# Kernel optimization log

Hardware: AMD Instinct MI355X
Metric: run time of the kernel (lower is better)

## Reference

```python
import jax, jax.numpy as jnp
import numpy as np
import math

D_PAIR = 64
N_HEADS = 4
D_HEAD = D_PAIR // N_HEADS


def setup_inputs() -> dict:
    key = jax.random.key(0)
    ks = jax.random.split(key, 9)
    B, L, D = 2, 256, D_PAIR
    s = 1.0 / math.sqrt(D)
    return {
        "z": jax.random.normal(ks[0], (B, L, L, D), dtype=jnp.float32),
        "ln_scale": jnp.ones((D,), jnp.float32),
        "ln_bias": jnp.zeros((D,), jnp.float32),
        "Wq": jax.random.normal(ks[1], (D, D), jnp.float32) * s,
        "Wk": jax.random.normal(ks[2], (D, D), jnp.float32) * s,
        "Wv": jax.random.normal(ks[3], (D, D), jnp.float32) * s,
        "Wg": jax.random.normal(ks[4], (D, D), jnp.float32) * s,
        "bg": jax.random.normal(ks[5], (D,), jnp.float32) * 0.02,
        "Wo": jax.random.normal(ks[6], (D, D), jnp.float32) * s,
        "bo": jax.random.normal(ks[7], (D,), jnp.float32) * 0.02,
    }


def _layernorm(x, scale, bias, eps=1e-5):
    mu = jnp.mean(x, axis=-1, keepdims=True)
    var = jnp.var(x, axis=-1, keepdims=True)
    return (x - mu) * jax.lax.rsqrt(var + eps) * scale + bias


def reference(z, ln_scale, ln_bias, Wq, Wk, Wv, Wg, bg, Wo, bo):
    B, L, _, D = z.shape
    H, Dh = N_HEADS, D_HEAD
    zn = _layernorm(z, ln_scale, ln_bias)
    # torch Linear(no bias): x @ W.T
    Q = (zn @ Wq.T).reshape(B, L, L, H, Dh)
    K = (zn @ Wk.T).reshape(B, L, L, H, Dh)
    V = (zn @ Wv.T).reshape(B, L, L, H, Dh)
    scale = 1.0 / math.sqrt(Dh)
    # row-wise attention: for each row l, attend over column index j
    attn = jnp.einsum("blihd,bljhd->blhij", Q, K) * scale  # [B,L,H,L,L]
    attn = jax.nn.softmax(attn, axis=-1)
    out = jnp.einsum("blhij,bljhd->blihd", attn, V).reshape(B, L, L, D)
    gate = jax.nn.sigmoid(zn @ Wg.T + bg)
    out = gate * out
    return out @ Wo.T + bo
```

## Files before the change

kernel.cpp:

```cpp
#include <hip/hip_runtime.h>
#include <hip/hip_bf16.h>
#include <math.h>


typedef __attribute__((ext_vector_type(4))) float f32x4;
typedef __attribute__((ext_vector_type(8))) short s16x8;
typedef __attribute__((ext_vector_type(4))) short s16x4;

#define MFMA16(a, b, c) __builtin_amdgcn_mfma_f32_16x16x32_bf16((a), (b), (c), 0, 0, 0)

__device__ __forceinline__ f32x4 mfma16b(s16x4 a, s16x4 b, f32x4 c) {
#if __has_builtin(__builtin_amdgcn_mfma_f32_16x16x16bf16_1k)
    return __builtin_amdgcn_mfma_f32_16x16x16bf16_1k(a, b, c, 0, 0, 0);
#elif __has_builtin(__builtin_amdgcn_mfma_f32_16x16x16_bf16)
    return __builtin_amdgcn_mfma_f32_16x16x16_bf16(a, b, c, 0, 0, 0);
#else
    f32x4 d;
    asm volatile("s_nop 1\n\t"
                 "v_mfma_f32_16x16x16_bf16 %0, %1, %2, %3\n\t"
                 "s_nop 7\n\t"
                 "s_nop 7"
                 : "=v"(d) : "v"(a), "v"(b), "v"(c));
    return d;
#endif
}

__device__ __forceinline__ float exp2a(float x) {
    float r;
    asm("v_exp_f32 %0, %1" : "=v"(r) : "v"(x));
    return r;
}
__device__ __forceinline__ float rcpa(float x) {
    float r;
    asm("v_rcp_f32 %0, %1" : "=v"(r) : "v"(x));
    return r;
}

__device__ __forceinline__ unsigned pk2(float a, float b) {
    union { __hip_bfloat162 h; unsigned u; } c;
    float2 t; t.x = a; t.y = b;
    c.h = __float22bfloat162_rn(t);
    return c.u;
}
__device__ __forceinline__ s16x8 cvt8(const float* p) {
    union { unsigned u[4]; s16x8 v; } r;
    r.u[0] = pk2(p[0], p[1]); r.u[1] = pk2(p[2], p[3]);
    r.u[2] = pk2(p[4], p[5]); r.u[3] = pk2(p[6], p[7]);
    return r.v;
}

static constexpr int WSLICE = 1024;
static constexpr int ZNL = 0;
static constexpr int KSH = 4096;
static constexpr int VT  = 9216;
static constexpr int LDS_EL = 13440;

__global__ __launch_bounds__(256, 3)
void ka_fused(const float* __restrict__ z, const float* __restrict__ ln_s,
              const float* __restrict__ ln_b, const float* __restrict__ Wq,
              const float* __restrict__ Wk, const float* __restrict__ Wv,
              const float* __restrict__ Wg, const float* __restrict__ bg,
              short* __restrict__ ws)
{
    __shared__ __align__(16) short lds[LDS_EL];
    const int tid = threadIdx.x, lane = tid & 63, w = tid >> 6;
    const int n16 = lane & 15, quad = lane >> 4;
    const int g = blockIdx.x, bl = g >> 2, h = g & 3;
    const size_t rowbase = (size_t)bl * (256 * 64);
    const int wsl = w * WSLICE;

    union { unsigned u[32]; s16x8 v8[8]; } row;
    {
        float zn[64];
        const float4* zp4 = (const float4*)(z + rowbase + (size_t)tid * 64);
        #pragma unroll
        for (int gq = 0; gq < 16; ++gq) {
            float4 v4 = zp4[gq];
            zn[gq * 4 + 0] = v4.x; zn[gq * 4 + 1] = v4.y;
            zn[gq * 4 + 2] = v4.z; zn[gq * 4 + 3] = v4.w;
        }
        float mu = 0.f;
        #pragma unroll
        for (int k = 0; k < 64; ++k) mu += zn[k];
        mu *= (1.f / 64.f);
        float va = 0.f;
        #pragma unroll
        for (int k = 0; k < 64; ++k) { float d = zn[k] - mu; va += d * d; }
        const float rs = rsqrtf(va * (1.f / 64.f) + 1e-5f);
        #pragma unroll
        for (int k = 0; k < 64; ++k) zn[k] = (zn[k] - mu) * rs * ln_s[k] + ln_b[k];
        #pragma unroll
        for (int k = 0; k < 32; ++k) row.u[k] = pk2(zn[2 * k], zn[2 * k + 1]);
    }

    auto store_row = [&]() {
        #pragma unroll
        for (int gq = 0; gq < 8; ++gq)
            *(s16x8*)&lds[ZNL + wsl + (lane & 15) * 64
                          + ((gq ^ (lane & 7)) * 8)] = row.v8[gq];
    };

    s16x8 bq[2], bk[2], bv[2], bgf[2];
    #pragma unroll
    for (int ks = 0; ks < 2; ++ks) {
        size_t off = (size_t)(h * 16 + n16) * 64 + ks * 32 + quad * 8;
        bq[ks] = cvt8(Wq + off);  bk[ks] = cvt8(Wk + off);
        bv[ks] = cvt8(Wv + off);  bgf[ks] = cvt8(Wg + off);
    }
    const float4 bg4 = *(const float4*)(bg + h * 16 + quad * 4);
    constexpr float QS  = 0.25f;
    constexpr float L2E = 1.44269504088896340736f;

    float g4t[4][4];
    s16x4 qa4[4];
    auto proj_tile = [&](int t) {
        s16x8 zn0 = *(const s16x8*)&lds[ZNL + wsl + n16 * 64
                                        + ((quad ^ (n16 & 7)) * 8)];
        s16x8 zn1 = *(const s16x8*)&lds[ZNL + wsl + n16 * 64
                                        + (((4 + quad) ^ (n16 & 7)) * 8)];
        f32x4 aq = {}, ak = {}, av = {}, ag = {};
        aq = MFMA16(bq[0], zn0, aq);  aq = MFMA16(bq[1], zn1, aq);
        ak = MFMA16(bk[0], zn0, ak);  ak = MFMA16(bk[1], zn1, ak);
        ag = MFMA16(bgf[0], zn0, ag); ag = MFMA16(bgf[1], zn1, ag);
        av = MFMA16(zn0, bv[0], av);  av = MFMA16(zn1, bv[1], av);
        {
            union { unsigned u[2]; s16x4 v; } q;
            q.u[0] = pk2(aq[0] * QS, aq[1] * QS);
            q.u[1] = pk2(aq[2] * QS, aq[3] * QS);
            qa4[t] = q.v;
        }
        {
            uint2 p = {pk2(ak[0], ak[1]), pk2(ak[2], ak[3])};
            *(uint2*)&lds[KSH + (w * 64 + t * 16 + n16) * 20 + quad * 4] = p;
        }
        {
            uint2 p = {pk2(av[0], av[1]), pk2(av[2], av[3])};
            *(uint2*)&lds[VT + n16 * 264 + (w * 64 + t * 16 + quad * 4)] = p;
        }
        #pragma unroll
        for (int r = 0; r < 4; ++r) {
            float x = ag[r] + bg4[r];
            g4t[t][r] = rcpa(1.f + exp2a(x * -L2E));
        }
    };

    if ((lane >> 4) == 0) store_row();
    proj_tile(0);
    if ((lane >> 4) == 1) store_row();
    proj_tile(1);
    if ((lane >> 4) == 2) store_row();
    proj_tile(2);
    if ((lane >> 4) == 3) store_row();
    proj_tile(3);
    __syncthreads();

    f32x4 o4[4], lacc[4];
    #pragma unroll
    for (int qt = 0; qt < 4; ++qt) { o4[qt] = {}; lacc[qt] = {}; }
    s16x4 ones4;
    {
        union { unsigned u[2]; s16x4 v; } c;
        c.u[0] = 0x3F803F80u; c.u[1] = 0x3F803F80u;
        ones4 = c.v;
    }
    const int kbase = KSH + n16 * 20 + quad * 4;
    const int vbase = VT + n16 * 264 + quad * 4;
    for (int ch = 0; ch < 8; ++ch) {
        #pragma unroll
        for (int jtl = 0; jtl < 2; ++jtl) {
            const int jt = ch * 2 + jtl;
            s16x4 kf = *(const s16x4*)&lds[kbase + jt * 320];
            s16x4 vf = *(const s16x4*)&lds[vbase + jt * 16];
            #pragma unroll
            for (int qt = 0; qt < 4; ++qt) {
                f32x4 zc = {};
                f32x4 s = mfma16b(kf, qa4[qt], zc);
                float e0 = exp2a(s[0] * L2E), e1 = exp2a(s[1] * L2E);
                float e2 = exp2a(s[2] * L2E), e3 = exp2a(s[3] * L2E);
                union { unsigned u[2]; s16x4 v; } pb;
                pb.u[0] = pk2(e0, e1); pb.u[1] = pk2(e2, e3);
                o4[qt]   = mfma16b(vf, pb.v, o4[qt]);
                lacc[qt] = mfma16b(ones4, pb.v, lacc[qt]);
            }
        }
    }

    #pragma unroll
    for (int qt = 0; qt < 4; ++qt) {
        const float l = (lacc[qt][0] + lacc[qt][1]) * 0.5f;
        const float inv = rcpa(l);
        float g0 = g4t[qt][0] * o4[qt][0] * inv;
        float g1 = g4t[qt][1] * o4[qt][1] * inv;
        float g2 = g4t[qt][2] * o4[qt][2] * inv;
        float g3 = g4t[qt][3] * o4[qt][3] * inv;
        uint2 p = {pk2(g0, g1), pk2(g2, g3)};
        short* dst = ws + (((size_t)h * 512 + bl) * 256 + w * 64 + qt * 16 + n16) * 16
                     + quad * 4;
        *(uint2*)dst = p;
    }
}

__global__ __launch_bounds__(256, 4)
void k3_out(const short* __restrict__ ws, const float* __restrict__ Wo,
            const float* __restrict__ bo, float* __restrict__ out)
{
    const int tid = threadIdx.x, lane = tid & 63, w = tid >> 6;
    const int n16 = lane & 15, quad = lane >> 4;
    const short* GO = ws;
    const int bl = blockIdx.x >> 1, half = blockIdx.x & 1;
    const int rowloc = half * 128 + w * 32;

    s16x8 bfr[4][2];
    #pragma unroll
    for (int nt = 0; nt < 4; ++nt)
        #pragma unroll
        for (int ks = 0; ks < 2; ++ks)
            bfr[nt][ks] = cvt8(Wo + (size_t)(nt * 16 + n16) * 64 + ks * 32 + quad * 8);

    f32x4 acc[2][4] = {};
    #pragma unroll
    for (int mt = 0; mt < 2; ++mt) {
        #pragma unroll
        for (int c = 0; c < 2; ++c) {
            int hp = c * 2 + (quad >> 1);
            const short* ap = &GO[(((size_t)hp * 512 + bl) * 256 + rowloc + mt * 16 + n16) * 16
                                  + (quad & 1) * 8];
            s16x8 a = *(const s16x8*)ap;
            #pragma unroll
            for (int nt = 0; nt < 4; ++nt)
                acc[mt][nt] = MFMA16(bfr[nt][c], a, acc[mt][nt]);
        }
    }
    #pragma unroll
    for (int nt = 0; nt < 4; ++nt) {
        const float4 b4 = *(const float4*)(bo + nt * 16 + quad * 4);
        f32x4 b4v; b4v[0] = b4.x; b4v[1] = b4.y; b4v[2] = b4.z; b4v[3] = b4.w;
        #pragma unroll
        for (int mt = 0; mt < 2; ++mt) {
            f32x4 v = acc[mt][nt] + b4v;
            *(f32x4*)&out[((size_t)bl * 256 + rowloc + mt * 16 + n16) * 64
                          + nt * 16 + quad * 4] = v;
        }
    }
}

extern "C" void kernel_launch(void* const* d_in, const int* in_sizes, int n_in,
                              void* d_out, int out_size, void* d_ws, size_t ws_size,
                              hipStream_t stream) {
    const float* z  = (const float*)d_in[0];
    const float* ls = (const float*)d_in[1];
    const float* lb = (const float*)d_in[2];
    const float* Wq = (const float*)d_in[3];
    const float* Wk = (const float*)d_in[4];
    const float* Wv = (const float*)d_in[5];
    const float* Wg = (const float*)d_in[6];
    const float* bg = (const float*)d_in[7];
    const float* Wo = (const float*)d_in[8];
    const float* bo = (const float*)d_in[9];
    float* out = (float*)d_out;
    short* wsp = (short*)d_ws;

    hipLaunchKernelGGL(ka_fused, dim3(2048), dim3(256), 0, stream,
                       z, ls, lb, Wq, Wk, Wv, Wg, bg, wsp);
    hipLaunchKernelGGL(k3_out, dim3(1024), dim3(256), 0, stream, wsp, Wo, bo, out);
}
```

Baseline: 149.8 us.

## Split LayerNorm into separate kernel writing bf16 normalized rows

Adds a k0_ln kernel that layer-normalizes each row once and stores it as bf16 in the output buffer, used as scratch. Before, each of the four head blocks re-read the fp32 z row and recomputed LayerNorm. The fused kernel now loads bf16 rows straight from global memory into the MFMA operands, drops the LDS staging area and reorders the block index so blocks for different heads of the same row sit farther apart. This cuts fp32 z traffic about fourfold and redundant LN math, at the cost of an extra launch and a bf16 round trip through global memory.

```diff
diff --git a/kernel.cpp b/kernel.cpp
--- a/kernel.cpp
+++ b/kernel.cpp
@@ -49,15 +49,43 @@
     return r.v;
 }
 
-static constexpr int WSLICE = 1024;
-static constexpr int ZNL = 0;
-static constexpr int KSH = 4096;
-static constexpr int VT  = 9216;
-static constexpr int LDS_EL = 13440;
+__global__ __launch_bounds__(256, 2)
+void k0_ln(const float* __restrict__ z, const float* __restrict__ ln_s,
+           const float* __restrict__ ln_b, short* __restrict__ znG)
+{
+    const size_t row = (size_t)blockIdx.x * 256 + threadIdx.x;
+    float zn[64];
+    const float4* zp4 = (const float4*)(z + row * 64);
+    #pragma unroll
+    for (int gq = 0; gq < 16; ++gq) {
+        float4 v4 = zp4[gq];
+        zn[gq * 4 + 0] = v4.x; zn[gq * 4 + 1] = v4.y;
+        zn[gq * 4 + 2] = v4.z; zn[gq * 4 + 3] = v4.w;
+    }
+    float mu = 0.f;
+    #pragma unroll
+    for (int k = 0; k < 64; ++k) mu += zn[k];
+    mu *= (1.f / 64.f);
+    float va = 0.f;
+    #pragma unroll
+    for (int k = 0; k < 64; ++k) { float d = zn[k] - mu; va += d * d; }
+    const float rs = rsqrtf(va * (1.f / 64.f) + 1e-5f);
+    #pragma unroll
+    for (int k = 0; k < 64; ++k) zn[k] = (zn[k] - mu) * rs * ln_s[k] + ln_b[k];
+    union { unsigned u[32]; uint4 q[8]; } pk;
+    #pragma unroll
+    for (int k = 0; k < 32; ++k) pk.u[k] = pk2(zn[2 * k], zn[2 * k + 1]);
+    uint4* dst = (uint4*)(znG + row * 64);
+    #pragma unroll
+    for (int i = 0; i < 8; ++i) dst[i] = pk.q[i];
+}
+
+static constexpr int KSH = 0;
+static constexpr int VT  = 5120;
+static constexpr int LDS_EL = 9344;
 
 __global__ __launch_bounds__(256, 3)
-void ka_fused(const float* __restrict__ z, const float* __restrict__ ln_s,
-              const float* __restrict__ ln_b, const float* __restrict__ Wq,
+void ka_fused(const short* __restrict__ znG, const float* __restrict__ Wq,
               const float* __restrict__ Wk, const float* __restrict__ Wv,
               const float* __restrict__ Wg, const float* __restrict__ bg,
               short* __restrict__ ws)
@@ -65,40 +93,8 @@
     __shared__ __align__(16) short lds[LDS_EL];
     const int tid = threadIdx.x, lane = tid & 63, w = tid >> 6;
     const int n16 = lane & 15, quad = lane >> 4;
-    const int g = blockIdx.x, bl = g >> 2, h = g & 3;
-    const size_t rowbase = (size_t)bl * (256 * 64);
-    const int wsl = w * WSLICE;
-
-    union { unsigned u[32]; s16x8 v8[8]; } row;
-    {
-        float zn[64];
-        const float4* zp4 = (const float4*)(z + rowbase + (size_t)tid * 64);
-        #pragma unroll
-        for (int gq = 0; gq < 16; ++gq) {
-            float4 v4 = zp4[gq];
-            zn[gq * 4 + 0] = v4.x; zn[gq * 4 + 1] = v4.y;
-            zn[gq * 4 + 2] = v4.z; zn[gq * 4 + 3] = v4.w;
-        }
-        float mu = 0.f;
-        #pragma unroll
-        for (int k = 0; k < 64; ++k) mu += zn[k];
-        mu *= (1.f / 64.f);
-        float va = 0.f;
-        #pragma unroll
-        for (int k = 0; k < 64; ++k) { float d = zn[k] - mu; va += d * d; }
-        const float rs = rsqrtf(va * (1.f / 64.f) + 1e-5f);
-        #pragma unroll
-        for (int k = 0; k < 64; ++k) zn[k] = (zn[k] - mu) * rs * ln_s[k] + ln_b[k];
-        #pragma unroll
-        for (int k = 0; k < 32; ++k) row.u[k] = pk2(zn[2 * k], zn[2 * k + 1]);
-    }
-
-    auto store_row = [&]() {
-        #pragma unroll
-        for (int gq = 0; gq < 8; ++gq)
-            *(s16x8*)&lds[ZNL + wsl + (lane & 15) * 64
-                          + ((gq ^ (lane & 7)) * 8)] = row.v8[gq];
-    };
+    const int g = blockIdx.x, bl = g & 511, h = g >> 9;
+    const int wsl_rows = w * 64;
 
     s16x8 bq[2], bk[2], bv[2], bgf[2];
     #pragma unroll
@@ -113,11 +109,12 @@
 
     float g4t[4][4];
     s16x4 qa4[4];
-    auto proj_tile = [&](int t) {
-        s16x8 zn0 = *(const s16x8*)&lds[ZNL + wsl + n16 * 64
-                                        + ((quad ^ (n16 & 7)) * 8)];
-        s16x8 zn1 = *(const s16x8*)&lds[ZNL + wsl + n16 * 64
-                                        + (((4 + quad) ^ (n16 & 7)) * 8)];
+    #pragma unroll
+    for (int t = 0; t < 4; ++t) {
+        const short* zr = znG + ((size_t)bl * 256 + wsl_rows + t * 16 + n16) * 64
+                          + quad * 8;
+        s16x8 zn0 = *(const s16x8*)zr;
+        s16x8 zn1 = *(const s16x8*)(zr + 32);
         f32x4 aq = {}, ak = {}, av = {}, ag = {};
         aq = MFMA16(bq[0], zn0, aq);  aq = MFMA16(bq[1], zn1, aq);
         ak = MFMA16(bk[0], zn0, ak);  ak = MFMA16(bk[1], zn1, ak);
@@ -131,27 +128,18 @@
         }
         {
             uint2 p = {pk2(ak[0], ak[1]), pk2(ak[2], ak[3])};
-            *(uint2*)&lds[KSH + (w * 64 + t * 16 + n16) * 20 + quad * 4] = p;
+            *(uint2*)&lds[KSH + (wsl_rows + t * 16 + n16) * 20 + quad * 4] = p;
         }
         {
             uint2 p = {pk2(av[0], av[1]), pk2(av[2], av[3])};
-            *(uint2*)&lds[VT + n16 * 264 + (w * 64 + t * 16 + quad * 4)] = p;
+            *(uint2*)&lds[VT + n16 * 264 + (wsl_rows + t * 16 + quad * 4)] = p;
         }
         #pragma unroll
         for (int r = 0; r < 4; ++r) {
             float x = ag[r] + bg4[r];
             g4t[t][r] = rcpa(1.f + exp2a(x * -L2E));
         }
-    };
-
-    if ((lane >> 4) == 0) store_row();
-    proj_tile(0);
-    if ((lane >> 4) == 1) store_row();
-    proj_tile(1);
-    if ((lane >> 4) == 2) store_row();
-    proj_tile(2);
-    if ((lane >> 4) == 3) store_row();
-    proj_tile(3);
+    }
     __syncthreads();
 
     f32x4 o4[4], lacc[4];
@@ -194,7 +182,7 @@
         float g2 = g4t[qt][2] * o4[qt][2] * inv;
         float g3 = g4t[qt][3] * o4[qt][3] * inv;
         uint2 p = {pk2(g0, g1), pk2(g2, g3)};
-        short* dst = ws + (((size_t)h * 512 + bl) * 256 + w * 64 + qt * 16 + n16) * 16
+        short* dst = ws + (((size_t)h * 512 + bl) * 256 + wsl_rows + qt * 16 + n16) * 16
                      + quad * 4;
         *(uint2*)dst = p;
     }
@@ -259,8 +247,10 @@
     const float* bo = (const float*)d_in[9];
     float* out = (float*)d_out;
     short* wsp = (short*)d_ws;
-
+    short* znG = (short*)d_out;
+
+    hipLaunchKernelGGL(k0_ln, dim3(512), dim3(256), 0, stream, z, ls, lb, znG);
     hipLaunchKernelGGL(ka_fused, dim3(2048), dim3(256), 0, stream,
-                       z, ls, lb, Wq, Wk, Wv, Wg, bg, wsp);
+                       znG, Wq, Wk, Wv, Wg, bg, wsp);
     hipLaunchKernelGGL(k3_out, dim3(1024), dim3(256), 0, stream, wsp, Wo, bo, out);
 }
```

Result: slower. 154.5 us (+3.1%).
